# Kernel optimization log

Hardware: AMD Instinct MI355X
Metric: run time of the kernel (lower is better)

The kernel has to match this reference:

```python
import jax, jax.numpy as jnp
import numpy as np

B, H, W, C = 2, 128, 128, 256
D = 64          # attention_dim
NH = 1          # num_heads
P = 18          # num_random_points
N = H * W
EPS = 1e-5


def _layernorm(x, gamma, beta):
    mu = jnp.mean(x, axis=-1, keepdims=True)
    var = jnp.var(x, axis=-1, keepdims=True)
    return (x - mu) * jax.lax.rsqrt(var + EPS) * gamma + beta


def setup_inputs() -> dict:
    key = jax.random.key(0)
    ks = jax.random.split(key, 12)
    s = 0.02
    inp = {
        "X": jax.random.normal(ks[0], (B, H, W, C), dtype=jnp.float32),
        "selected_indices": jax.random.randint(ks[1], (B, N, P), 0, N),
        "topk": 1,
        "pos_enc": jax.random.normal(ks[2], (1, H, W, C), dtype=jnp.float32),
        "Wq": jax.random.normal(ks[3], (C, NH * D), dtype=jnp.float32) * s,
        "bq": jnp.zeros((NH * D,), dtype=jnp.float32),
        "Wk": jax.random.normal(ks[4], (C, NH * D), dtype=jnp.float32) * s,
        "bk": jnp.zeros((NH * D,), dtype=jnp.float32),
        "Wv": jax.random.normal(ks[5], (C, NH * D), dtype=jnp.float32) * s,
        "bv": jnp.zeros((NH * D,), dtype=jnp.float32),
        "Wo": jax.random.normal(ks[6], (NH * D, C), dtype=jnp.float32) * s,
        "bo": jnp.zeros((C,), dtype=jnp.float32),
        "W1": jax.random.normal(ks[7], (C, 4 * C), dtype=jnp.float32) * s,
        "b1": jnp.zeros((4 * C,), dtype=jnp.float32),
        "W2": jax.random.normal(ks[8], (4 * C, C), dtype=jnp.float32) * s,
        "b2": jnp.zeros((C,), dtype=jnp.float32),
        "g1": jnp.ones((C,), dtype=jnp.float32),
        "be1": jnp.zeros((C,), dtype=jnp.float32),
        "g2": jnp.ones((C,), dtype=jnp.float32),
        "be2": jnp.zeros((C,), dtype=jnp.float32),
    }
    return inp


def reference(X, selected_indices, topk, pos_enc, Wq, bq, Wk, bk, Wv, bv,
              Wo, bo, W1, b1, W2, b2, g1, be1, g2, be2):
    # forward_wotopk path (topk == 1)
    Xp = X + pos_enc                                  # [B,H,W,C]
    Q = (Xp @ Wq + bq).reshape(B, N, NH, D)
    K = (Xp @ Wk + bk).reshape(B, N, NH, D)
    V = (Xp @ Wv + bv).reshape(B, N, NH, D)

    # gather 18 random K/V rows per query pixel: [B,N,P,NH,D]
    gather = jax.vmap(lambda kv, idx: kv[idx])        # per-batch fancy index
    Ksel = gather(K, selected_indices)
    Vsel = gather(V, selected_indices)

    scores = jnp.einsum('bihd,bijhd->bijh', Q, Ksel) / jnp.sqrt(
        jnp.asarray(D, dtype=jnp.float32))
    attn = jax.nn.softmax(scores, axis=2)             # softmax over the P points
    ctx = jnp.einsum('bijh,bijhd->bihd', attn, Vsel).reshape(B, N, NH * D)

    out = (ctx @ Wo + bo).reshape(B, H, W, C)
    Xn = _layernorm(Xp + out, g1, be1)
    ffn = jax.nn.relu(Xn @ W1 + b1) @ W2 + b2
    out2 = _layernorm(Xn + ffn, g2, be2)
    return out2, attn
```

## Files before the change

### kernel.cpp

```cpp
#include <hip/hip_runtime.h>
#include <hip/hip_bf16.h>

#define CC 256
#define DD 64
#define PP 18
#define ROWS 32768
#define EPSF 1e-5f

typedef __attribute__((ext_vector_type(8))) short bf16x8;
typedef __attribute__((ext_vector_type(4))) short s16x4;
typedef __attribute__((ext_vector_type(4))) float f32x4;

#define WAIT_VM(N) do {                                       \
    asm volatile("s_waitcnt vmcnt(" #N ")" ::: "memory");     \
    __builtin_amdgcn_s_barrier();                             \
    __builtin_amdgcn_sched_barrier(0);                        \
} while (0)

__device__ __forceinline__ void gl_lds16(const void* g, void* l) {
    __builtin_amdgcn_global_load_lds(
        (const __attribute__((address_space(1))) unsigned int*)g,
        (__attribute__((address_space(3))) unsigned int*)l, 16, 0, 0);
}

__device__ __forceinline__ void inv_swz(int p, int& r, int& c) {
    int rhi = p >> 7;
    int r2  = (rhi >> 1) & 1;
    int r0  = ((p >> 6) & 1) ^ r2;
    r = (rhi << 1) | r0;
    c = ((p >> 4) & 3) ^ (r & 3);
}

__global__ __launch_bounds__(256) void k_prep(
    const float* __restrict__ Wq, const float* __restrict__ Wk,
    const float* __restrict__ Wv, const float* __restrict__ Wo,
    const float* __restrict__ W1, const float* __restrict__ W2,
    __hip_bfloat16* __restrict__ WqP, __hip_bfloat16* __restrict__ WkP,
    __hip_bfloat16* __restrict__ WvP, __hip_bfloat16* __restrict__ WoP,
    __hip_bfloat16* __restrict__ W1T, __hip_bfloat16* __restrict__ W2T) {
    __shared__ float tile[32][33];
    const int b = blockIdx.x, t = threadIdx.x;
    if (b < 256) {
        int i = b * 256 + t;
        const float* src; __hip_bfloat16* dst; int K, N, j;
        if (i < 16384)      { src = Wq; dst = WqP; K = 256; N = 64;  j = i; }
        else if (i < 32768) { src = Wk; dst = WkP; K = 256; N = 64;  j = i - 16384; }
        else if (i < 49152) { src = Wv; dst = WvP; K = 256; N = 64;  j = i - 32768; }
        else                { src = Wo; dst = WoP; K = 64;  N = 256; j = i - 49152; }
        int e = j & 7, l = (j >> 3) & 63, rest = j >> 9;
        int KS = K >> 5;
        int ks = rest % KS, nt = rest / KS;
        int row = ks * 32 + (l >> 4) * 8 + e;
        int col = nt * 16 + (l & 15);
        dst[j] = __float2bfloat16(src[(long)row * N + col]);
        return;
    }
    const float* src; __hip_bfloat16* dst; int Nsrc, r0, c0, mode;
    if (b < 512) {
        int bb = b - 256;
        r0 = (bb >> 5) * 32; c0 = (bb & 31) * 32;
        src = W1; dst = W1T; Nsrc = 1024; mode = 0;
    } else {
        int bb = b - 512;
        r0 = (bb >> 3) * 32; c0 = (bb & 7) * 32;
        src = W2; dst = W2T; Nsrc = 256; mode = 1;
    }
#pragma unroll
    for (int i = 0; i < 4; ++i) {
        int idx = t + i * 256;
        int r = idx >> 5, c = idx & 31;
        tile[r][c] = src[(long)(r0 + r) * Nsrc + c0 + c];
    }
    __syncthreads();
#pragma unroll
    for (int i = 0; i < 4; ++i) {
        int idx = t + i * 256;
        int c2 = idx >> 5, r2 = idx & 31;
        long doff = (mode == 0) ? ((long)(c0 + c2) * 256 + r0 + r2)
                                : ((long)(c0 + c2) * 1024 + r0 + r2);
        dst[doff] = __float2bfloat16(tile[r2][c2]);
    }
}

__global__ __launch_bounds__(256) void k_qkv(
    const float4* __restrict__ X4, const float4* __restrict__ pe4,
    const __hip_bfloat16* __restrict__ WqP, const __hip_bfloat16* __restrict__ WkP,
    const __hip_bfloat16* __restrict__ WvP,
    const float* __restrict__ bq, const float* __restrict__ bk,
    const float* __restrict__ bv,
    __hip_bfloat16* __restrict__ Xpb,
    __hip_bfloat16* __restrict__ Qb, __hip_bfloat16* __restrict__ Kb,
    __hip_bfloat16* __restrict__ Vb) {
    __shared__ short Xs[32 * 256];
    const int t = threadIdx.x, w = t >> 6, l = t & 63;
    const int l15 = l & 15, lh = l >> 4;
    const int row0 = blockIdx.x * 32;

    for (int j = t; j < 2048; j += 256) {
        int r = j >> 6, c4 = j & 63;
        long g = row0 + r;
        float4 a = X4[(g << 6) + c4];
        float4 p = pe4[(long)((g & 16383) << 6) + c4];
        union { s16x4 v; __hip_bfloat16 h[4]; } u;
        u.h[0] = __float2bfloat16(a.x + p.x);
        u.h[1] = __float2bfloat16(a.y + p.y);
        u.h[2] = __float2bfloat16(a.z + p.z);
        u.h[3] = __float2bfloat16(a.w + p.w);
        int db = (r << 9) + (c4 << 3);
        db ^= (r & 7) << 4;
        *(s16x4*)((char*)Xs + db) = u.v;
        *(s16x4*)((char*)Xpb + (g << 9) + (c4 << 3)) = u.v;
    }
    __syncthreads();

    bf16x8 af[2][8];
#pragma unroll
    for (int ri = 0; ri < 2; ++ri)
#pragma unroll
        for (int ks = 0; ks < 8; ++ks) {
            int r = ri * 16 + l15;
            int db = (r << 9) + ks * 64 + lh * 16;
            db ^= (r & 7) << 4;
            af[ri][ks] = *(const bf16x8*)((const char*)Xs + db);
        }

    f32x4 acc[3][2];
#pragma unroll
    for (int j = 0; j < 3; ++j)
#pragma unroll
        for (int ri = 0; ri < 2; ++ri) acc[j][ri] = (f32x4)(0.f);

#pragma unroll
    for (int ks = 0; ks < 8; ++ks)
#pragma unroll
        for (int j = 0; j < 3; ++j) {
            int nt = w * 3 + j;
            const __hip_bfloat16* WP = (nt < 4) ? WqP : ((nt < 8) ? WkP : WvP);
            int ntl = nt & 3;
            bf16x8 b = *(const bf16x8*)(WP + (long)(((ntl * 8 + ks) << 6) + l) * 8);
#pragma unroll
            for (int ri = 0; ri < 2; ++ri)
                acc[j][ri] = __builtin_amdgcn_mfma_f32_16x16x32_bf16(
                    af[ri][ks], b, acc[j][ri], 0, 0, 0);
        }

#pragma unroll
    for (int j = 0; j < 3; ++j) {
        int nt = w * 3 + j;
        __hip_bfloat16* OP = (nt < 4) ? Qb : ((nt < 8) ? Kb : Vb);
        const float* BP = (nt < 4) ? bq : ((nt < 8) ? bk : bv);
        int col = (nt & 3) * 16 + l15;
        float bias = BP[col];
#pragma unroll
        for (int ri = 0; ri < 2; ++ri)
#pragma unroll
            for (int rg = 0; rg < 4; ++rg) {
                long row = row0 + ri * 16 + lh * 4 + rg;
                OP[row * DD + col] = __float2bfloat16(acc[j][ri][rg] + bias);
            }
    }
}

__global__ __launch_bounds__(256) void k_attn(const __hip_bfloat16* __restrict__ Q,
                                              const __hip_bfloat16* __restrict__ K,
                                              const __hip_bfloat16* __restrict__ V,
                                              const int* __restrict__ sel,
                                              __hip_bfloat16* __restrict__ ctx,
                                              float* __restrict__ attn_out) {
    const int wave  = threadIdx.x >> 6;
    const int lane  = threadIdx.x & 63;
    const int token = blockIdx.x * 4 + wave;
    const int b     = token >> 14;
    const int g = lane >> 3, s = lane & 7;

    const int* selp = sel + (long)token * PP;
    int sel_l = (lane < PP) ? selp[lane] : 0;

    float qf[8];
    {
        uint4 qv = *(const uint4*)(Q + (long)token * DD + s * 8);
        qf[0] = __uint_as_float(qv.x << 16);
        qf[1] = __uint_as_float(qv.x & 0xffff0000u);
        qf[2] = __uint_as_float(qv.y << 16);
        qf[3] = __uint_as_float(qv.y & 0xffff0000u);
        qf[4] = __uint_as_float(qv.z << 16);
        qf[5] = __uint_as_float(qv.z & 0xffff0000u);
        qf[6] = __uint_as_float(qv.w << 16);
        qf[7] = __uint_as_float(qv.w & 0xffff0000u);
    }

    const __hip_bfloat16* Kbase = K + (((long)b << 14) * DD);
    float sc[3];
    int idxs[3];
#pragma unroll
    for (int i = 0; i < 3; ++i) {
        int r = i * 8 + g;
        idxs[i] = __shfl(sel_l, r);
        uint4 kv = *(const uint4*)(Kbase + (long)idxs[i] * DD + s * 8);
        float part;
        part = qf[0] * __uint_as_float(kv.x << 16);
        part = fmaf(qf[1], __uint_as_float(kv.x & 0xffff0000u), part);
        part = fmaf(qf[2], __uint_as_float(kv.y << 16), part);
        part = fmaf(qf[3], __uint_as_float(kv.y & 0xffff0000u), part);
        part = fmaf(qf[4], __uint_as_float(kv.z << 16), part);
        part = fmaf(qf[5], __uint_as_float(kv.z & 0xffff0000u), part);
        part = fmaf(qf[6], __uint_as_float(kv.w << 16), part);
        part = fmaf(qf[7], __uint_as_float(kv.w & 0xffff0000u), part);
        part += __shfl_xor(part, 1);
        part += __shfl_xor(part, 2);
        part += __shfl_xor(part, 4);
        sc[i] = (r < PP) ? part * 0.125f : -1e30f;
    }

    float m = fmaxf(fmaxf(sc[0], sc[1]), sc[2]);
    m = fmaxf(m, __shfl_xor(m, 8));
    m = fmaxf(m, __shfl_xor(m, 16));
    m = fmaxf(m, __shfl_xor(m, 32));
    const float L2E = 1.4426950408889634f;
    float e0 = exp2f((sc[0] - m) * L2E);
    float e1 = exp2f((sc[1] - m) * L2E);
    float e2 = exp2f((sc[2] - m) * L2E);
    float dsum = e0 + e1 + e2;
    dsum += __shfl_xor(dsum, 8);
    dsum += __shfl_xor(dsum, 16);
    dsum += __shfl_xor(dsum, 32);
    float inv = 1.f / dsum;

    {
        int srcl = (lane & 7) << 3;
        float b0 = __shfl(e0, srcl);
        float b1 = __shfl(e1, srcl);
        float b2 = __shfl(e2, srcl);
        if (lane < PP) {
            float ev = (lane < 8) ? b0 : ((lane < 16) ? b1 : b2);
            attn_out[(long)token * PP + lane] = ev * inv;
        }
    }

    const __hip_bfloat16* Vbase = V + (((long)b << 14) * DD);
    float ca[8];
#pragma unroll
    for (int j = 0; j < 8; ++j) ca[j] = 0.f;
    float ev3[3] = {e0, e1, e2};
#pragma unroll
    for (int i = 0; i < 3; ++i) {
        uint4 vv = *(const uint4*)(Vbase + (long)idxs[i] * DD + s * 8);
        float e = ev3[i];
        ca[0] = fmaf(e, __uint_as_float(vv.x << 16), ca[0]);
        ca[1] = fmaf(e, __uint_as_float(vv.x & 0xffff0000u), ca[1]);
        ca[2] = fmaf(e, __uint_as_float(vv.y << 16), ca[2]);
        ca[3] = fmaf(e, __uint_as_float(vv.y & 0xffff0000u), ca[3]);
        ca[4] = fmaf(e, __uint_as_float(vv.z << 16), ca[4]);
        ca[5] = fmaf(e, __uint_as_float(vv.z & 0xffff0000u), ca[5]);
        ca[6] = fmaf(e, __uint_as_float(vv.w << 16), ca[6]);
        ca[7] = fmaf(e, __uint_as_float(vv.w & 0xffff0000u), ca[7]);
    }
#pragma unroll
    for (int o = 8; o <= 32; o <<= 1)
#pragma unroll
        for (int j = 0; j < 8; ++j) ca[j] += __shfl_xor(ca[j], o);
    if (g == 0) {
        union { bf16x8 v; __hip_bfloat16 h[8]; } u;
#pragma unroll
        for (int j = 0; j < 8; ++j) u.h[j] = __float2bfloat16(ca[j] * inv);
        *(bf16x8*)(ctx + (long)token * DD + s * 8) = u.v;
    }
}

__global__ __launch_bounds__(256) void k_projln(
    const __hip_bfloat16* __restrict__ ctx, const __hip_bfloat16* __restrict__ WoP,
    const float* __restrict__ bo, const float* __restrict__ g1,
    const float* __restrict__ be1,
    const __hip_bfloat16* __restrict__ Xpb, __hip_bfloat16* __restrict__ Xnb) {
    __shared__ short Cs[32 * 64];
    __shared__ float red[2][32][2];
    __shared__ float mrs[32][2];
    const int t = threadIdx.x, w = t >> 6, l = t & 63;
    const int l15 = l & 15, lh = l >> 4;
    const int row0 = blockIdx.x * 32;

    {
        int r = t >> 3, ch = t & 7;
        int db = (r << 7) + (ch << 4);
        db ^= (r & 7) << 4;
        *(bf16x8*)((char*)Cs + db) = *(const bf16x8*)(ctx + (long)(row0 + r) * DD + ch * 8);
    }
    __syncthreads();

    const int ri = w & 1, nh = w >> 1;

    bf16x8 af[2];
#pragma unroll
    for (int ks = 0; ks < 2; ++ks) {
        int r = ri * 16 + l15;
        int db = (r << 7) + ks * 64 + lh * 16;
        db ^= (r & 7) << 4;
        af[ks] = *(const bf16x8*)((const char*)Cs + db);
    }

    f32x4 acc[8];
#pragma unroll
    for (int j = 0; j < 8; ++j) acc[j] = (f32x4)(0.f);

#pragma unroll
    for (int ks = 0; ks < 2; ++ks)
#pragma unroll
        for (int j = 0; j < 8; ++j) {
            int nt = nh * 8 + j;
            bf16x8 b = *(const bf16x8*)(WoP + (long)(((nt * 2 + ks) << 6) + l) * 8);
            acc[j] = __builtin_amdgcn_mfma_f32_16x16x32_bf16(af[ks], b, acc[j], 0, 0, 0);
        }

    float bov[8], g1v[8], be1v[8];
#pragma unroll
    for (int j = 0; j < 8; ++j) {
        int col = (nh * 8 + j) * 16 + l15;
        bov[j] = bo[col]; g1v[j] = g1[col]; be1v[j] = be1[col];
    }

    float xv[4][8];
#pragma unroll
    for (int rg = 0; rg < 4; ++rg) {
        long grow = row0 + ri * 16 + lh * 4 + rg;
        float s = 0.f, q = 0.f;
#pragma unroll
        for (int j = 0; j < 8; ++j) {
            float v = acc[j][rg] + bov[j] +
                      __bfloat162float(Xpb[grow * CC + (nh * 8 + j) * 16 + l15]);
            xv[rg][j] = v; s += v; q += v * v;
        }
#pragma unroll
        for (int o = 8; o > 0; o >>= 1) { s += __shfl_xor(s, o); q += __shfl_xor(q, o); }
        if (l15 == 0) {
            int rl = ri * 16 + lh * 4 + rg;
            red[nh][rl][0] = s; red[nh][rl][1] = q;
        }
    }
    __syncthreads();
    if (t < 32) {
        float S = red[0][t][0] + red[1][t][0];
        float Q = red[0][t][1] + red[1][t][1];
        float mu = S * (1.f / CC);
        float var = Q * (1.f / CC) - mu * mu;
        mrs[t][0] = mu; mrs[t][1] = rsqrtf(var + EPSF);
    }
    __syncthreads();
#pragma unroll
    for (int rg = 0; rg < 4; ++rg) {
        int rl = ri * 16 + lh * 4 + rg;
        long grow = row0 + rl;
        float mu = mrs[rl][0], rs = mrs[rl][1];
#pragma unroll
        for (int j = 0; j < 8; ++j)
            Xnb[grow * CC + (nh * 8 + j) * 16 + l15] =
                __float2bfloat16((xv[rg][j] - mu) * rs * g1v[j] + be1v[j]);
    }
}

template<int KD, int NDIM, int GRL2, int CTL2>
__global__ __launch_bounds__(256) void k_gemm(
    const __hip_bfloat16* __restrict__ A,
    const __hip_bfloat16* __restrict__ BT,
    const float* __restrict__ bias,
    __hip_bfloat16* __restrict__ Cout) {
    __shared__ short As[4][4096];
    __shared__ short Bs[4][4096];

    const int t = threadIdx.x, w = t >> 6, l = t & 63;
    const int l15 = l & 15, lh = l >> 4;
    const int bid = blockIdx.x;
    const int wi = bid & ((1 << (GRL2 + CTL2)) - 1);
    const int rt = ((bid >> (GRL2 + CTL2)) << GRL2) | (wi & ((1 << GRL2) - 1));
    const int ct = wi >> GRL2;
    const int row0 = rt * 128, n0 = ct * 128;
    const int wr = w & 1, wc = w >> 1;

    const __hip_bfloat16* gA[2];
    const __hip_bfloat16* gB[2];
#pragma unroll
    for (int j = 0; j < 2; ++j) {
        int r, c;
        inv_swz(j * 4096 + t * 16, r, c);
        gA[j] = A  + (long)(row0 + r) * KD + c * 8;
        gB[j] = BT + (long)(n0 + r) * KD + c * 8;
    }
    char* ldsA = (char*)As + w * 1024;
    char* ldsB = (char*)Bs + w * 1024;

    int offA[4], offB[4];
#pragma unroll
    for (int f = 0; f < 4; ++f) {
        int rowA = wr * 64 + f * 16 + l15;
        offA[f] = (rowA * 64 + lh * 16) ^ ((rowA & 7) << 4);
        int rowB = wc * 64 + f * 16 + l15;
        offB[f] = (rowB * 64 + lh * 16) ^ ((rowB & 7) << 4);
    }

    f32x4 acc[4][4];
#pragma unroll
    for (int i = 0; i < 4; ++i)
#pragma unroll
        for (int j = 0; j < 4; ++j) acc[i][j] = (f32x4)(0.f);

    constexpr int KS = KD / 32;
#pragma unroll
    for (int n = 0; n < 3; ++n)
#pragma unroll
        for (int j = 0; j < 2; ++j) {
            gl_lds16(gA[j] + n * 32, ldsA + n * 8192 + j * 4096);
            gl_lds16(gB[j] + n * 32, ldsB + n * 8192 + j * 4096);
        }

#pragma unroll 1
    for (int ks = 0; ks < KS; ++ks) {
        if (ks + 2 < KS)      { WAIT_VM(8); }
        else if (ks + 1 < KS) { WAIT_VM(4); }
        else                  { WAIT_VM(0); }
        if (ks + 3 < KS) {
            int nb = (ks + 3) & 3;
#pragma unroll
            for (int j = 0; j < 2; ++j) {
                gl_lds16(gA[j] + (ks + 3) * 32, ldsA + nb * 8192 + j * 4096);
                gl_lds16(gB[j] + (ks + 3) * 32, ldsB + nb * 8192 + j * 4096);
            }
        }
        const char* as = (const char*)As + (ks & 3) * 8192;
        const char* bs = (const char*)Bs + (ks & 3) * 8192;
        bf16x8 af[4], bfr[4];
#pragma unroll
        for (int f = 0; f < 4; ++f)
            af[f] = *(const bf16x8*)(as + offA[f]);
#pragma unroll
        for (int f = 0; f < 4; ++f)
            bfr[f] = *(const bf16x8*)(bs + offB[f]);
#pragma unroll
        for (int fr = 0; fr < 4; ++fr)
#pragma unroll
            for (int fc = 0; fc < 4; ++fc)
                acc[fr][fc] = __builtin_amdgcn_mfma_f32_16x16x32_bf16(
                    af[fr], bfr[fc], acc[fr][fc], 0, 0, 0);
    }

#pragma unroll
    for (int fc = 0; fc < 4; ++fc) {
        int col = n0 + wc * 64 + fc * 16 + l15;
        float bv = bias[col];
#pragma unroll
        for (int fr = 0; fr < 4; ++fr)
#pragma unroll
            for (int rg = 0; rg < 4; ++rg) {
                int row = wr * 64 + fr * 16 + lh * 4 + rg;
                long gi = (long)(row0 + row) * NDIM + col;
                Cout[gi] = __float2bfloat16(fmaxf(acc[fr][fc][rg] + bv, 0.f));
            }
    }
}

__global__ __launch_bounds__(512) void k_gemm2ln(
    const __hip_bfloat16* __restrict__ A,
    const __hip_bfloat16* __restrict__ BT,
    const float* __restrict__ b2,
    const __hip_bfloat16* __restrict__ Res,
    const float* __restrict__ g2, const float* __restrict__ be2,
    float* __restrict__ out) {
    __shared__ short As[3][2048];
    __shared__ short Bs[3][8192];
    __shared__ float red[4][64][2];
    __shared__ float mrs[64][2];

    const int t = threadIdx.x, w = t >> 6, l = t & 63;
    const int l15 = l & 15, lh = l >> 4;
    const int wr = w >> 2, wc = w & 3;
    const int row0 = blockIdx.x * 64;
    const bool doA = (t < 256);

    const __hip_bfloat16* gA = A;
    {
        int r, c;
        inv_swz((t & 255) * 16, r, c);
        gA = A + (long)(row0 + r) * 1024 + c * 8;
    }
    const __hip_bfloat16* gB[2];
#pragma unroll
    for (int j = 0; j < 2; ++j) {
        int r, c;
        inv_swz(j * 8192 + t * 16, r, c);
        gB[j] = BT + (long)r * 1024 + c * 8;
    }
    char* ldsA = (char*)As + (w & 3) * 1024;
    char* ldsB = (char*)Bs + w * 1024;

    int offA[2], offB[4];
#pragma unroll
    for (int f = 0; f < 2; ++f) {
        int rowA = wr * 32 + f * 16 + l15;
        offA[f] = (rowA * 64 + lh * 16) ^ ((rowA & 7) << 4);
    }
#pragma unroll
    for (int f = 0; f < 4; ++f) {
        int rowB = wc * 64 + f * 16 + l15;
        offB[f] = (rowB * 64 + lh * 16) ^ ((rowB & 7) << 4);
    }

    f32x4 acc[2][4];
#pragma unroll
    for (int i = 0; i < 2; ++i)
#pragma unroll
        for (int j = 0; j < 4; ++j) acc[i][j] = (f32x4)(0.f);

#pragma unroll
    for (int n = 0; n < 2; ++n) {
        if (doA) gl_lds16(gA + n * 32, ldsA + n * 4096);
#pragma unroll
        for (int j = 0; j < 2; ++j)
            gl_lds16(gB[j] + n * 32, ldsB + n * 16384 + j * 8192);
    }

    int cb = 0;
#pragma unroll 1
    for (int ks = 0; ks < 32; ++ks) {
        if (ks + 1 < 32) {
            if (doA) asm volatile("s_waitcnt vmcnt(3)" ::: "memory");
            else     asm volatile("s_waitcnt vmcnt(2)" ::: "memory");
            __builtin_amdgcn_s_barrier();
            __builtin_amdgcn_sched_barrier(0);
        } else {
            WAIT_VM(0);
        }
        if (ks + 2 < 32) {
            int ib = cb + 2; if (ib >= 3) ib -= 3;
            if (doA) gl_lds16(gA + (ks + 2) * 32, ldsA + ib * 4096);
#pragma unroll
            for (int j = 0; j < 2; ++j)
                gl_lds16(gB[j] + (ks + 2) * 32, ldsB + ib * 16384 + j * 8192);
        }
        const char* as = (const char*)As + cb * 4096;
        const char* bs = (const char*)Bs + cb * 16384;
        bf16x8 af[2], bfr[4];
#pragma unroll
        for (int f = 0; f < 2; ++f)
            af[f] = *(const bf16x8*)(as + offA[f]);
#pragma unroll
        for (int f = 0; f < 4; ++f)
            bfr[f] = *(const bf16x8*)(bs + offB[f]);
#pragma unroll
        for (int fr = 0; fr < 2; ++fr)
#pragma unroll
            for (int fc = 0; fc < 4; ++fc)
                acc[fr][fc] = __builtin_amdgcn_mfma_f32_16x16x32_bf16(
                    af[fr], bfr[fc], acc[fr][fc], 0, 0, 0);
        if (++cb == 3) cb = 0;
    }

    float b2v[4], g2v[4], be2v[4];
#pragma unroll
    for (int fc = 0; fc < 4; ++fc) {
        int col = wc * 64 + fc * 16 + l15;
        b2v[fc] = b2[col]; g2v[fc] = g2[col]; be2v[fc] = be2[col];
    }
#pragma unroll
    for (int fr = 0; fr < 2; ++fr)
#pragma unroll
        for (int rg = 0; rg < 4; ++rg) {
            int row = wr * 32 + fr * 16 + lh * 4 + rg;
            float s = 0.f, q = 0.f;
#pragma unroll
            for (int fc = 0; fc < 4; ++fc) {
                long gi = (long)(row0 + row) * CC + wc * 64 + fc * 16 + l15;
                float v = acc[fr][fc][rg] + b2v[fc] + __bfloat162float(Res[gi]);
                acc[fr][fc][rg] = v;
                s += v; q += v * v;
            }
#pragma unroll
            for (int o = 8; o > 0; o >>= 1) {
                s += __shfl_xor(s, o); q += __shfl_xor(q, o);
            }
            if (l15 == 0) { red[wc][row][0] = s; red[wc][row][1] = q; }
        }
    __syncthreads();
    if (t < 64) {
        float S = 0.f, Q = 0.f;
#pragma unroll
        for (int ww = 0; ww < 4; ++ww) { S += red[ww][t][0]; Q += red[ww][t][1]; }
        float mu = S * (1.f / CC);
        float var = Q * (1.f / CC) - mu * mu;
        mrs[t][0] = mu; mrs[t][1] = rsqrtf(var + EPSF);
    }
    __syncthreads();
#pragma unroll
    for (int fr = 0; fr < 2; ++fr)
#pragma unroll
        for (int rg = 0; rg < 4; ++rg) {
            int row = wr * 32 + fr * 16 + lh * 4 + rg;
            float mu = mrs[row][0], rs = mrs[row][1];
#pragma unroll
            for (int fc = 0; fc < 4; ++fc) {
                long gi = (long)(row0 + row) * CC + wc * 64 + fc * 16 + l15;
                out[gi] = (acc[fr][fc][rg] - mu) * rs * g2v[fc] + be2v[fc];
            }
        }
}

extern "C" void kernel_launch(void* const* d_in, const int* in_sizes, int n_in,
                              void* d_out, int out_size, void* d_ws, size_t ws_size,
                              hipStream_t stream) {
    const float* X   = (const float*)d_in[0];
    const int*   sel = (const int*)d_in[1];
    const float* pe  = (const float*)d_in[3];
    const float* Wq  = (const float*)d_in[4];
    const float* bq  = (const float*)d_in[5];
    const float* Wk  = (const float*)d_in[6];
    const float* bk  = (const float*)d_in[7];
    const float* Wv  = (const float*)d_in[8];
    const float* bv  = (const float*)d_in[9];
    const float* Wo  = (const float*)d_in[10];
    const float* bo  = (const float*)d_in[11];
    const float* W1  = (const float*)d_in[12];
    const float* b1  = (const float*)d_in[13];
    const float* W2  = (const float*)d_in[14];
    const float* b2  = (const float*)d_in[15];
    const float* g1  = (const float*)d_in[16];
    const float* be1 = (const float*)d_in[17];
    const float* g2  = (const float*)d_in[18];
    const float* be2 = (const float*)d_in[19];

    float* out = (float*)d_out;
    char*  ws  = (char*)d_ws;

    __hip_bfloat16* Xpb = (__hip_bfloat16*)(ws);
    __hip_bfloat16* Qb  = (__hip_bfloat16*)(ws + (16 << 20));
    __hip_bfloat16* Kb  = (__hip_bfloat16*)(ws + (20 << 20));
    __hip_bfloat16* Vb  = (__hip_bfloat16*)(ws + (24 << 20));
    __hip_bfloat16* ctxb= (__hip_bfloat16*)(ws + (28 << 20));
    __hip_bfloat16* H   = (__hip_bfloat16*)(ws + (16 << 20));
    __hip_bfloat16* WqP = (__hip_bfloat16*)(ws + (96 << 20));
    __hip_bfloat16* WkP = WqP + 16384;
    __hip_bfloat16* WvP = WkP + 16384;
    __hip_bfloat16* WoP = WvP + 16384;
    __hip_bfloat16* W1T = WoP + 16384;
    __hip_bfloat16* W2T = W1T + 262144;
    float* attn_out = out + (long)ROWS * CC;

    k_prep<<<768, 256, 0, stream>>>(Wq, Wk, Wv, Wo, W1, W2,
                                    WqP, WkP, WvP, WoP, W1T, W2T);

    k_qkv<<<ROWS / 32, 256, 0, stream>>>((const float4*)X, (const float4*)pe,
                                         WqP, WkP, WvP, bq, bk, bv,
                                         Xpb, Qb, Kb, Vb);

    k_attn<<<ROWS / 4, 256, 0, stream>>>(Qb, Kb, Vb, sel, ctxb, attn_out);

    k_projln<<<ROWS / 32, 256, 0, stream>>>(ctxb, WoP, bo, g1, be1, Xpb, Xpb);

    k_gemm<256, 1024, 3, 3><<<2048, 256, 0, stream>>>(Xpb, W1T, b1, H);
    k_gemm2ln<<<512, 512, 0, stream>>>(H, W2T, b2, Xpb, g2, be2, out);
}
```

Before: 124.9 us.

## Retile FFN GEMMs: 128x256 tiles for GEMM1, K=64 double-buffered steps for GEMM2

The first FFN GEMM now uses 512-thread blocks computing 128x256 output tiles with a 3-stage LDS pipeline instead of 256-thread 128x128 tiles with 4 stages, which halves the block count and raises A-tile reuse. The second GEMM+LayerNorm kernel now loads K=64 slices per step with 128-byte swizzled rows and double buffering. In that kernel, fragments are read into registers before the next prefetch is issued into the same buffer, and the LDS reduction scratch is aliased onto the A buffer. Together these cut barrier count and loop overhead, at the cost of more LDS per block, lower pipeline depth and possibly lower occupancy.

```diff
diff --git a/kernel.cpp b/kernel.cpp
--- a/kernel.cpp
+++ b/kernel.cpp
@@ -29,6 +29,11 @@
     int r0  = ((p >> 6) & 1) ^ r2;
     r = (rhi << 1) | r0;
     c = ((p >> 4) & 3) ^ (r & 3);
+}
+
+__device__ __forceinline__ void inv_swz128(int p, int& r, int& c) {
+    r = p >> 7;
+    c = ((p >> 4) & 7) ^ (r & 7);
 }
 
 __global__ __launch_bounds__(256) void k_prep(
@@ -358,13 +363,13 @@
 }
 
 template<int KD, int NDIM, int GRL2, int CTL2>
-__global__ __launch_bounds__(256) void k_gemm(
+__global__ __launch_bounds__(512) void k_gemm1(
     const __hip_bfloat16* __restrict__ A,
     const __hip_bfloat16* __restrict__ BT,
     const float* __restrict__ bias,
     __hip_bfloat16* __restrict__ Cout) {
-    __shared__ short As[4][4096];
-    __shared__ short Bs[4][4096];
+    __shared__ short As[3][4096];
+    __shared__ short Bs[3][8192];
 
     const int t = threadIdx.x, w = t >> 6, l = t & 63;
     const int l15 = l & 15, lh = l >> 4;
@@ -372,16 +377,16 @@
     const int wi = bid & ((1 << (GRL2 + CTL2)) - 1);
     const int rt = ((bid >> (GRL2 + CTL2)) << GRL2) | (wi & ((1 << GRL2) - 1));
     const int ct = wi >> GRL2;
-    const int row0 = rt * 128, n0 = ct * 128;
-    const int wr = w & 1, wc = w >> 1;
-
-    const __hip_bfloat16* gA[2];
+    const int row0 = rt * 128, n0 = ct * 256;
+    const int wr = w >> 2, wc = w & 3;
+
+    const __hip_bfloat16* gA;
+    { int r, c; inv_swz(t * 16, r, c); gA = A + (long)(row0 + r) * KD + c * 8; }
     const __hip_bfloat16* gB[2];
 #pragma unroll
     for (int j = 0; j < 2; ++j) {
         int r, c;
-        inv_swz(j * 4096 + t * 16, r, c);
-        gA[j] = A  + (long)(row0 + r) * KD + c * 8;
+        inv_swz(j * 8192 + t * 16, r, c);
         gB[j] = BT + (long)(n0 + r) * KD + c * 8;
     }
     char* ldsA = (char*)As + w * 1024;
@@ -404,28 +409,26 @@
 
     constexpr int KS = KD / 32;
 #pragma unroll
-    for (int n = 0; n < 3; ++n)
-#pragma unroll
-        for (int j = 0; j < 2; ++j) {
-            gl_lds16(gA[j] + n * 32, ldsA + n * 8192 + j * 4096);
-            gl_lds16(gB[j] + n * 32, ldsB + n * 8192 + j * 4096);
-        }
-
+    for (int n = 0; n < 2; ++n) {
+        gl_lds16(gA + n * 32, ldsA + n * 8192);
+#pragma unroll
+        for (int j = 0; j < 2; ++j)
+            gl_lds16(gB[j] + n * 32, ldsB + n * 16384 + j * 8192);
+    }
+
+    int cb = 0;
 #pragma unroll 1
     for (int ks = 0; ks < KS; ++ks) {
-        if (ks + 2 < KS)      { WAIT_VM(8); }
-        else if (ks + 1 < KS) { WAIT_VM(4); }
-        else                  { WAIT_VM(0); }
-        if (ks + 3 < KS) {
-            int nb = (ks + 3) & 3;
-#pragma unroll
-            for (int j = 0; j < 2; ++j) {
-                gl_lds16(gA[j] + (ks + 3) * 32, ldsA + nb * 8192 + j * 4096);
-                gl_lds16(gB[j] + (ks + 3) * 32, ldsB + nb * 8192 + j * 4096);
-            }
-        }
-        const char* as = (const char*)As + (ks & 3) * 8192;
-        const char* bs = (const char*)Bs + (ks & 3) * 8192;
+        if (ks + 1 < KS) { WAIT_VM(3); } else { WAIT_VM(0); }
+        if (ks + 2 < KS) {
+            int ib = cb + 2; if (ib >= 3) ib -= 3;
+            gl_lds16(gA + (ks + 2) * 32, ldsA + ib * 8192);
+#pragma unroll
+            for (int j = 0; j < 2; ++j)
+                gl_lds16(gB[j] + (ks + 2) * 32, ldsB + ib * 16384 + j * 8192);
+        }
+        const char* as = (const char*)As + cb * 8192;
+        const char* bs = (const char*)Bs + cb * 16384;
         bf16x8 af[4], bfr[4];
 #pragma unroll
         for (int f = 0; f < 4; ++f)
@@ -439,6 +442,7 @@
             for (int fc = 0; fc < 4; ++fc)
                 acc[fr][fc] = __builtin_amdgcn_mfma_f32_16x16x32_bf16(
                     af[fr], bfr[fc], acc[fr][fc], 0, 0, 0);
+        if (++cb == 3) cb = 0;
     }
 
 #pragma unroll
@@ -463,43 +467,44 @@
     const __hip_bfloat16* __restrict__ Res,
     const float* __restrict__ g2, const float* __restrict__ be2,
     float* __restrict__ out) {
-    __shared__ short As[3][2048];
-    __shared__ short Bs[3][8192];
-    __shared__ float red[4][64][2];
-    __shared__ float mrs[64][2];
+    __shared__ short As[2][4096];
+    __shared__ short Bs[2][16384];
+    float* red = (float*)As;
+    float* mrs = (float*)As + 512;
 
     const int t = threadIdx.x, w = t >> 6, l = t & 63;
     const int l15 = l & 15, lh = l >> 4;
     const int wr = w >> 2, wc = w & 3;
     const int row0 = blockIdx.x * 64;
-    const bool doA = (t < 256);
-
-    const __hip_bfloat16* gA = A;
-    {
+
+    const __hip_bfloat16* gA;
+    { int r, c; inv_swz128(t * 16, r, c); gA = A + (long)(row0 + r) * 1024 + c * 8; }
+    const __hip_bfloat16* gB[4];
+#pragma unroll
+    for (int j = 0; j < 4; ++j) {
         int r, c;
-        inv_swz((t & 255) * 16, r, c);
-        gA = A + (long)(row0 + r) * 1024 + c * 8;
-    }
-    const __hip_bfloat16* gB[2];
-#pragma unroll
-    for (int j = 0; j < 2; ++j) {
-        int r, c;
-        inv_swz(j * 8192 + t * 16, r, c);
+        inv_swz128(j * 8192 + t * 16, r, c);
         gB[j] = BT + (long)r * 1024 + c * 8;
     }
-    char* ldsA = (char*)As + (w & 3) * 1024;
+    char* ldsA = (char*)As + w * 1024;
     char* ldsB = (char*)Bs + w * 1024;
 
-    int offA[2], offB[4];
+    int offA[2][2], offB[4][2];
 #pragma unroll
     for (int f = 0; f < 2; ++f) {
         int rowA = wr * 32 + f * 16 + l15;
-        offA[f] = (rowA * 64 + lh * 16) ^ ((rowA & 7) << 4);
+        int sw = (rowA & 7) << 4;
+#pragma unroll
+        for (int kk = 0; kk < 2; ++kk)
+            offA[f][kk] = rowA * 128 + ((kk * 64 + lh * 16) ^ sw);
     }
 #pragma unroll
     for (int f = 0; f < 4; ++f) {
         int rowB = wc * 64 + f * 16 + l15;
-        offB[f] = (rowB * 64 + lh * 16) ^ ((rowB & 7) << 4);
+        int sw = (rowB & 7) << 4;
+#pragma unroll
+        for (int kk = 0; kk < 2; ++kk)
+            offB[f][kk] = rowB * 128 + ((kk * 64 + lh * 16) ^ sw);
     }
 
     f32x4 acc[2][4];
@@ -510,46 +515,45 @@
 
 #pragma unroll
     for (int n = 0; n < 2; ++n) {
-        if (doA) gl_lds16(gA + n * 32, ldsA + n * 4096);
-#pragma unroll
-        for (int j = 0; j < 2; ++j)
-            gl_lds16(gB[j] + n * 32, ldsB + n * 16384 + j * 8192);
-    }
-
-    int cb = 0;
+        gl_lds16(gA + n * 64, ldsA + n * 8192);
+#pragma unroll
+        for (int j = 0; j < 4; ++j)
+            gl_lds16(gB[j] + n * 64, ldsB + n * 32768 + j * 8192);
+    }
+
 #pragma unroll 1
-    for (int ks = 0; ks < 32; ++ks) {
-        if (ks + 1 < 32) {
-            if (doA) asm volatile("s_waitcnt vmcnt(3)" ::: "memory");
-            else     asm volatile("s_waitcnt vmcnt(2)" ::: "memory");
-            __builtin_amdgcn_s_barrier();
-            __builtin_amdgcn_sched_barrier(0);
-        } else {
-            WAIT_VM(0);
-        }
-        if (ks + 2 < 32) {
-            int ib = cb + 2; if (ib >= 3) ib -= 3;
-            if (doA) gl_lds16(gA + (ks + 2) * 32, ldsA + ib * 4096);
-#pragma unroll
-            for (int j = 0; j < 2; ++j)
-                gl_lds16(gB[j] + (ks + 2) * 32, ldsB + ib * 16384 + j * 8192);
-        }
-        const char* as = (const char*)As + cb * 4096;
-        const char* bs = (const char*)Bs + cb * 16384;
-        bf16x8 af[2], bfr[4];
+    for (int ks = 0; ks < 16; ++ks) {
+        if (ks + 1 < 16) { WAIT_VM(5); } else { WAIT_VM(0); }
+        const char* as = (const char*)As + (ks & 1) * 8192;
+        const char* bs = (const char*)Bs + (ks & 1) * 32768;
+        bf16x8 afr[2][2], bfr[4][2];
 #pragma unroll
         for (int f = 0; f < 2; ++f)
-            af[f] = *(const bf16x8*)(as + offA[f]);
+#pragma unroll
+            for (int kk = 0; kk < 2; ++kk)
+                afr[f][kk] = *(const bf16x8*)(as + offA[f][kk]);
 #pragma unroll
         for (int f = 0; f < 4; ++f)
-            bfr[f] = *(const bf16x8*)(bs + offB[f]);
-#pragma unroll
-        for (int fr = 0; fr < 2; ++fr)
-#pragma unroll
-            for (int fc = 0; fc < 4; ++fc)
-                acc[fr][fc] = __builtin_amdgcn_mfma_f32_16x16x32_bf16(
-                    af[fr], bfr[fc], acc[fr][fc], 0, 0, 0);
-        if (++cb == 3) cb = 0;
+#pragma unroll
+            for (int kk = 0; kk < 2; ++kk)
+                bfr[f][kk] = *(const bf16x8*)(bs + offB[f][kk]);
+        asm volatile("s_waitcnt lgkmcnt(0)" ::: "memory");
+        __builtin_amdgcn_s_barrier();
+        __builtin_amdgcn_sched_barrier(0);
+        if (ks + 2 < 16) {
+            gl_lds16(gA + (ks + 2) * 64, ldsA + (ks & 1) * 8192);
+#pragma unroll
+            for (int j = 0; j < 4; ++j)
+                gl_lds16(gB[j] + (ks + 2) * 64, ldsB + (ks & 1) * 32768 + j * 8192);
+        }
+#pragma unroll
+        for (int kk = 0; kk < 2; ++kk)
+#pragma unroll
+            for (int fr = 0; fr < 2; ++fr)
+#pragma unroll
+                for (int fc = 0; fc < 4; ++fc)
+                    acc[fr][fc] = __builtin_amdgcn_mfma_f32_16x16x32_bf16(
+                        afr[fr][kk], bfr[fc][kk], acc[fr][fc], 0, 0, 0);
     }
 
     float b2v[4], g2v[4], be2v[4];
@@ -558,6 +562,7 @@
         int col = wc * 64 + fc * 16 + l15;
         b2v[fc] = b2[col]; g2v[fc] = g2[col]; be2v[fc] = be2[col];
     }
+    __syncthreads();
 #pragma unroll
     for (int fr = 0; fr < 2; ++fr)
 #pragma unroll
@@ -575,16 +580,22 @@
             for (int o = 8; o > 0; o >>= 1) {
                 s += __shfl_xor(s, o); q += __shfl_xor(q, o);
             }
-            if (l15 == 0) { red[wc][row][0] = s; red[wc][row][1] = q; }
+            if (l15 == 0) {
+                red[(wc * 64 + row) * 2 + 0] = s;
+                red[(wc * 64 + row) * 2 + 1] = q;
+            }
         }
     __syncthreads();
     if (t < 64) {
         float S = 0.f, Q = 0.f;
 #pragma unroll
-        for (int ww = 0; ww < 4; ++ww) { S += red[ww][t][0]; Q += red[ww][t][1]; }
+        for (int ww = 0; ww < 4; ++ww) {
+            S += red[(ww * 64 + t) * 2 + 0];
+            Q += red[(ww * 64 + t) * 2 + 1];
+        }
         float mu = S * (1.f / CC);
         float var = Q * (1.f / CC) - mu * mu;
-        mrs[t][0] = mu; mrs[t][1] = rsqrtf(var + EPSF);
+        mrs[t * 2 + 0] = mu; mrs[t * 2 + 1] = rsqrtf(var + EPSF);
     }
     __syncthreads();
 #pragma unroll
@@ -592,7 +603,7 @@
 #pragma unroll
         for (int rg = 0; rg < 4; ++rg) {
             int row = wr * 32 + fr * 16 + lh * 4 + rg;
-            float mu = mrs[row][0], rs = mrs[row][1];
+            float mu = mrs[row * 2 + 0], rs = mrs[row * 2 + 1];
 #pragma unroll
             for (int fc = 0; fc < 4; ++fc) {
                 long gi = (long)(row0 + row) * CC + wc * 64 + fc * 16 + l15;
@@ -652,6 +663,6 @@
 
     k_projln<<<ROWS / 32, 256, 0, stream>>>(ctxb, WoP, bo, g1, be1, Xpb, Xpb);
 
-    k_gemm<256, 1024, 3, 3><<<2048, 256, 0, stream>>>(Xpb, W1T, b1, H);
+    k_gemm1<256, 1024, 2, 2><<<1024, 512, 0, stream>>>(Xpb, W1T, b1, H);
     k_gemm2ln<<<512, 512, 0, stream>>>(H, W2T, b2, Xpb, g2, be2, out);
 }
```

Result: faster. 114.8 us (-8.1%).
